# Performance work log

Measured on AMD Instinct MI355X. Metric: run time of the kernel, lower is better.

The kernel has to match this reference:

```python
import jax, jax.numpy as jnp
import numpy as np

D_DYN, D_STAT, H, T, B = 3, 3, 256, 365, 1024


def setup_inputs() -> dict:
    key = jax.random.key(0)
    ks = jax.random.split(key, 8)
    C = D_DYN + H
    s = lambda k, shape: jax.random.normal(k, shape, dtype=jnp.float32) * 0.05
    return {
        "x_dyn": jax.random.normal(ks[0], (B, T, D_DYN), dtype=jnp.float32),
        "x_stat": jax.random.normal(ks[1], (B, D_STAT), dtype=jnp.float32),
        "w_i": s(ks[2], (D_STAT, H)), "b_i": jnp.zeros((H,), jnp.float32),
        "w_f": s(ks[3], (C, H)), "b_f": jnp.zeros((H,), jnp.float32),
        "w_g": s(ks[4], (C, H)), "b_g": jnp.zeros((H,), jnp.float32),
        "w_o": s(ks[5], (C, H)), "b_o": jnp.zeros((H,), jnp.float32),
        "w_head": s(ks[6], (H, 1)), "b_head": jnp.zeros((1,), jnp.float32),
    }


def reference(x_dyn, x_stat, w_i, b_i, w_f, b_f, w_g, b_g, w_o, b_o, w_head, b_head):
    # Static input gate (EA-LSTM): i depends only on static features.
    i = jax.nn.sigmoid(x_stat @ w_i + b_i)  # (B, H)

    # Merge the three gate linears into one (C, 3H) matmul per step and
    # split the concat [x_t, h] into x- and h-parts (equivalent to torch.cat).
    W = jnp.concatenate([w_f, w_g, w_o], axis=1)  # (C, 3H)
    Wx, Wh = W[:D_DYN], W[D_DYN:]                 # (D,3H), (H,3H)
    b = jnp.concatenate([b_f, b_g, b_o])          # (3H,)

    def step(carry, x_t):
        h, c = carry
        z = x_t @ Wx + h @ Wh + b                 # (B, 3H)
        f = jax.nn.sigmoid(z[:, :H])
        g = jnp.tanh(z[:, H:2 * H])
        o = jax.nn.sigmoid(z[:, 2 * H:])
        c = f * c + i * g
        h = o * jnp.tanh(c)
        return (h, c), None

    h0 = jnp.zeros((x_dyn.shape[0], H), x_dyn.dtype)
    c0 = jnp.zeros((x_dyn.shape[0], H), x_dyn.dtype)
    (h, _), _ = jax.lax.scan(step, (h0, c0), jnp.swapaxes(x_dyn, 0, 1))
    # Dropout is identity in eval mode.
    return h @ w_head + b_head  # (B, 1)
```

## Files before the change

### kernel.cpp

```cpp
#include <hip/hip_runtime.h>
#include <hip/hip_bf16.h>

#define T_STEPS 365
#define XLEN    (T_STEPS * 3)
#define H_SZ    256
#define ROWS    16
#define NW      8
#define CPW     32

#define SF1     (-1.4426950408889634f)
#define SF2     (-2.8853900817779268f)

typedef __attribute__((ext_vector_type(8))) short bf16x8;
typedef __attribute__((ext_vector_type(4))) short bf16x4;
typedef __attribute__((ext_vector_type(4))) float f32x4;

__device__ __forceinline__ float fast_sigmoid(float x) {
    return __builtin_amdgcn_rcpf(1.0f + __builtin_amdgcn_exp2f(-1.44269504f * x));
}
__device__ __forceinline__ unsigned short f2bf(float x) {
    __hip_bfloat16 b = __float2bfloat16(x);
    return *reinterpret_cast<unsigned short*>(&b);
}
__device__ __forceinline__ float bf2f(unsigned short v) {
    return __uint_as_float(((unsigned)v) << 16);
}
__device__ __forceinline__ bf16x8 expand4(bf16x4 v) {
    bf16x8 r = (bf16x8)0;
    r[0] = v[0]; r[1] = v[1]; r[2] = v[2]; r[3] = v[3];
    return r;
}

__global__ void __launch_bounds__(256)
xstage(const float* __restrict__ x_dyn, unsigned short* __restrict__ xg)
{
    const int rb = blockIdx.x * ROWS;
    for (int idx = threadIdx.x; idx < T_STEPS * ROWS; idx += 256) {
        const int t = idx % T_STEPS, r = idx / T_STEPS;
        const float* s = x_dyn + (size_t)(rb + r) * XLEN + t * 3;
        bf16x4 pk;
        pk[0] = (short)f2bf(s[0]); pk[1] = (short)f2bf(s[1]);
        pk[2] = (short)f2bf(s[2]); pk[3] = (short)0x3F80;
        *(bf16x4*)&xg[((size_t)blockIdx.x * T_STEPS + t) * 64 + r * 4] = pk;
    }
}

__global__ void __launch_bounds__(512, 2)
ealstm_fused(const unsigned short* __restrict__ xg, const float* __restrict__ x_stat,
             const float* __restrict__ w_i, const float* __restrict__ b_i,
             const float* __restrict__ w_f, const float* __restrict__ b_f,
             const float* __restrict__ w_g, const float* __restrict__ b_g,
             const float* __restrict__ w_o, const float* __restrict__ b_o,
             const float* __restrict__ w_head, const float* __restrict__ b_head,
             float* __restrict__ out)
{
    const int tid   = threadIdx.x;
    const int lane  = tid & 63;
    const int wv    = tid >> 6;
    const int m     = lane & 15;
    const int l16   = lane >> 4;
    const int rb    = blockIdx.x * ROWS;
    const int wbase = wv * CPW;

    __shared__ unsigned short wo_lds[4 * 8 * 256 * 8];
    __shared__ unsigned short hbuf[2][4096];
    __shared__ float          red[NW][ROWS];

    for (int idx = tid; idx < 4 * 8 * 8 * 256; idx += 512) {
        const int c    = idx & 255;
        const int e    = (idx >> 8) & 7;
        const int kt   = (idx >> 11) & 7;
        const int l16g = idx >> 14;
        wo_lds[((l16g * 8 + kt) * 256 + c) * 8 + e] =
            f2bf(SF1 * w_o[(3 + kt * 32 + l16g * 8 + e) * H_SZ + c]);
    }
    for (int idx = tid; idx < 2048; idx += 512) ((unsigned int*)hbuf[0])[idx] = 0u;

    const float* wsrc[3] = {w_f, w_g, w_o};
    const float* bsrc[3] = {b_f, b_g, b_o};
    const float  gsf[3]  = {SF1, SF2, SF1};

    bf16x8 wA[8][2][2];
    bf16x8 wXe[2][3];
#pragma unroll
    for (int ct = 0; ct < 2; ++ct) {
        const int c = wbase + ct * 16 + m;
#pragma unroll
        for (int g = 0; g < 2; ++g)
#pragma unroll
            for (int kt = 0; kt < 8; ++kt) {
                bf16x8 a;
#pragma unroll
                for (int e = 0; e < 8; ++e)
                    a[e] = (short)f2bf(gsf[g] * wsrc[g][(3 + kt * 32 + l16 * 8 + e) * H_SZ + c]);
                wA[kt][ct][g] = a;
            }
#pragma unroll
        for (int g = 0; g < 3; ++g) {
            bf16x4 ax = (bf16x4)0;
            if (l16 == 0) {
                ax[0] = (short)f2bf(gsf[g] * wsrc[g][0 * H_SZ + c]);
                ax[1] = (short)f2bf(gsf[g] * wsrc[g][1 * H_SZ + c]);
                ax[2] = (short)f2bf(gsf[g] * wsrc[g][2 * H_SZ + c]);
                ax[3] = (short)f2bf(gsf[g] * bsrc[g][c]);
            }
            wXe[ct][g] = expand4(ax);
        }
    }

    float iv[2][4], cst[2][4];
    {
        const float xs0 = x_stat[(rb + m) * 3 + 0];
        const float xs1 = x_stat[(rb + m) * 3 + 1];
        const float xs2 = x_stat[(rb + m) * 3 + 2];
#pragma unroll
        for (int ct = 0; ct < 2; ++ct)
#pragma unroll
            for (int q = 0; q < 4; ++q) {
                const int c = wbase + ct * 16 + l16 * 4 + q;
                iv[ct][q] = fast_sigmoid(b_i[c] + xs0 * w_i[c] + xs1 * w_i[H_SZ + c]
                                                + xs2 * w_i[2 * H_SZ + c]);
                cst[ct][q] = 0.0f;
            }
    }

    int woff[2];
#pragma unroll
    for (int ct = 0; ct < 2; ++ct) {
        const int c0 = wbase + ct * 16 + l16 * 4;
        woff[ct] = ((c0 >> 5) * 64 + m + 16 * ((c0 & 31) >> 3)) * 8 + (c0 & 7);
    }

    const unsigned short* xrow   = xg + (size_t)blockIdx.x * T_STEPS * 64 + m * 4;
    const bf16x8*         wobase = (const bf16x8*)&wo_lds[((l16 * 8) * 256 + wbase + m) * 8];

    __syncthreads();

    for (int t = 0; t < T_STEPS; ++t) {
        const int cur = t & 1;
        const bf16x8* hp = (const bf16x8*)hbuf[cur] + lane;
        unsigned short* hw = hbuf[cur ^ 1];

        bf16x8 xf = (bf16x8)0;
        {
            unsigned long long xv = *(const unsigned long long*)&xrow[(size_t)t * 64];
            if (l16 != 0) xv = 0ULL;
            union { unsigned long long u; bf16x4 v; } X; X.u = xv;
            xf[0] = X.v[0]; xf[1] = X.v[1]; xf[2] = X.v[2]; xf[3] = X.v[3];
        }
        bf16x8 hb[8];
#pragma unroll
        for (int kt = 0; kt < 8; ++kt) hb[kt] = hp[kt * 64];
        bf16x8 wor[8][2];
#pragma unroll
        for (int kt = 0; kt < 8; ++kt) {
            wor[kt][0] = wobase[kt * 256];
            wor[kt][1] = wobase[kt * 256 + 16];
        }

        f32x4 acc[2][3];
        {
            const f32x4 z4 = {0.f, 0.f, 0.f, 0.f};
#pragma unroll
            for (int ct = 0; ct < 2; ++ct)
#pragma unroll
                for (int g = 0; g < 3; ++g)
                    acc[ct][g] = __builtin_amdgcn_mfma_f32_16x16x32_bf16(
                        wXe[ct][g], xf, z4, 0, 0, 0);
        }

#pragma unroll
        for (int kt = 0; kt < 8; ++kt) {
            acc[0][0] = __builtin_amdgcn_mfma_f32_16x16x32_bf16(wA[kt][0][0], hb[kt], acc[0][0], 0, 0, 0);
            acc[0][1] = __builtin_amdgcn_mfma_f32_16x16x32_bf16(wA[kt][0][1], hb[kt], acc[0][1], 0, 0, 0);
            acc[0][2] = __builtin_amdgcn_mfma_f32_16x16x32_bf16(wor[kt][0],   hb[kt], acc[0][2], 0, 0, 0);
            acc[1][0] = __builtin_amdgcn_mfma_f32_16x16x32_bf16(wA[kt][1][0], hb[kt], acc[1][0], 0, 0, 0);
            acc[1][1] = __builtin_amdgcn_mfma_f32_16x16x32_bf16(wA[kt][1][1], hb[kt], acc[1][1], 0, 0, 0);
            acc[1][2] = __builtin_amdgcn_mfma_f32_16x16x32_bf16(wor[kt][1],   hb[kt], acc[1][2], 0, 0, 0);
        }

#pragma unroll
        for (int ct = 0; ct < 2; ++ct) {
            bf16x4 pk;
#pragma unroll
            for (int q = 0; q < 4; ++q) {
                const float Ef = __builtin_amdgcn_exp2f(acc[ct][0][q]);
                const float Eg = __builtin_amdgcn_exp2f(acc[ct][1][q]);
                const float Eo = __builtin_amdgcn_exp2f(acc[ct][2][q]);
                const float u  = 1.0f + Eg;
                const float v  = 1.0f + Ef;
                const float t2 = iv[ct][q] * (2.0f - u);
                const float cq = (cst[ct][q] * u + t2 * v) *
                                 __builtin_amdgcn_rcpf(u * v);
                cst[ct][q] = cq;
                const float Ec = __builtin_amdgcn_exp2f(SF2 * cq);
                const float hq = (1.0f - Ec) *
                                 __builtin_amdgcn_rcpf((1.0f + Eo) * (1.0f + Ec));
                pk[q] = (short)f2bf(hq);
            }
            *(bf16x4*)&hw[woff[ct]] = pk;
        }
        __syncthreads();
    }

    float p = 0.0f;
    const unsigned short* hf = hbuf[1];
#pragma unroll
    for (int ct = 0; ct < 2; ++ct) {
        const int c0 = wbase + ct * 16 + l16 * 4;
        const f32x4 wh = *(const f32x4*)&w_head[c0];
        const bf16x4 hv = *(const bf16x4*)&hf[woff[ct]];
#pragma unroll
        for (int q = 0; q < 4; ++q) p += bf2f((unsigned short)hv[q]) * wh[q];
    }
    p += __shfl_xor(p, 16);
    p += __shfl_xor(p, 32);
    if (lane < 16) red[wv][m] = p;
    __syncthreads();
    if (tid < ROWS) {
        float s = b_head[0];
#pragma unroll
        for (int w = 0; w < NW; ++w) s += red[w][tid];
        out[rb + tid] = s;
    }
}

extern "C" void kernel_launch(void* const* d_in, const int* in_sizes, int n_in,
                              void* d_out, int out_size, void* d_ws, size_t ws_size,
                              hipStream_t stream)
{
    const float* x_dyn  = (const float*)d_in[0];
    const float* x_stat = (const float*)d_in[1];
    const float* w_i    = (const float*)d_in[2];
    const float* b_i    = (const float*)d_in[3];
    const float* w_f    = (const float*)d_in[4];
    const float* b_f    = (const float*)d_in[5];
    const float* w_g    = (const float*)d_in[6];
    const float* b_g    = (const float*)d_in[7];
    const float* w_o    = (const float*)d_in[8];
    const float* b_o    = (const float*)d_in[9];
    const float* w_head = (const float*)d_in[10];
    const float* b_head = (const float*)d_in[11];

    unsigned short* xg = (unsigned short*)d_ws;

    xstage<<<dim3(64), dim3(256), 0, stream>>>(x_dyn, xg);
    ealstm_fused<<<dim3(64), dim3(512), 0, stream>>>(
        xg, x_stat, w_i, b_i, w_f, b_f, w_g, b_g, w_o, b_o,
        w_head, b_head, (float*)d_out);
}
```

Measured before the change: 578.1 us.

## Halve batch rows per block to 8 and double block count to 128

Each block now handles 8 batch rows instead of 16, and twice as many blocks are launched, so more CUs work on the sequential recurrence at once. The 16-wide MFMA N dimension stays the same, so half of each matmul's columns are padding. Lanes 8-15 take the second column tile's results through a cross-lane shuffle, which halves the per-lane gate elementwise work. The cost is wasted MFMA throughput, an extra shuffle step per timestep, and weight staging into registers and LDS repeated in twice as many blocks.

```diff
diff --git a/kernel.cpp b/kernel.cpp
--- a/kernel.cpp
+++ b/kernel.cpp
@@ -4,7 +4,8 @@
 #define T_STEPS 365
 #define XLEN    (T_STEPS * 3)
 #define H_SZ    256
-#define ROWS    16
+#define ROWS    8
+#define NBLK    128
 #define NW      8
 #define CPW     32
 
@@ -41,7 +42,7 @@
         bf16x4 pk;
         pk[0] = (short)f2bf(s[0]); pk[1] = (short)f2bf(s[1]);
         pk[2] = (short)f2bf(s[2]); pk[3] = (short)0x3F80;
-        *(bf16x4*)&xg[((size_t)blockIdx.x * T_STEPS + t) * 64 + r * 4] = pk;
+        *(bf16x4*)&xg[((size_t)blockIdx.x * T_STEPS + t) * 32 + r * 4] = pk;
     }
 }
 
@@ -61,6 +62,9 @@
     const int l16   = lane >> 4;
     const int rb    = blockIdx.x * ROWS;
     const int wbase = wv * CPW;
+    const int r_eff  = m & 7;
+    const int ct_eff = m >> 3;
+    const bool hi    = (m >= 8);
 
     __shared__ unsigned short wo_lds[4 * 8 * 256 * 8];
     __shared__ unsigned short hbuf[2][4096];
@@ -74,7 +78,7 @@
         wo_lds[((l16g * 8 + kt) * 256 + c) * 8 + e] =
             f2bf(SF1 * w_o[(3 + kt * 32 + l16g * 8 + e) * H_SZ + c]);
     }
-    for (int idx = tid; idx < 2048; idx += 512) ((unsigned int*)hbuf[0])[idx] = 0u;
+    for (int idx = tid; idx < 4096; idx += 512) ((unsigned int*)hbuf)[idx] = 0u;
 
     const float* wsrc[3] = {w_f, w_g, w_o};
     const float* bsrc[3] = {b_f, b_g, b_o};
@@ -108,30 +112,24 @@
         }
     }
 
-    float iv[2][4], cst[2][4];
+    const int c0 = wbase + ct_eff * 16 + l16 * 4;
+    float iv[4], cst[4];
     {
-        const float xs0 = x_stat[(rb + m) * 3 + 0];
-        const float xs1 = x_stat[(rb + m) * 3 + 1];
-        const float xs2 = x_stat[(rb + m) * 3 + 2];
-#pragma unroll
-        for (int ct = 0; ct < 2; ++ct)
-#pragma unroll
-            for (int q = 0; q < 4; ++q) {
-                const int c = wbase + ct * 16 + l16 * 4 + q;
-                iv[ct][q] = fast_sigmoid(b_i[c] + xs0 * w_i[c] + xs1 * w_i[H_SZ + c]
-                                                + xs2 * w_i[2 * H_SZ + c]);
-                cst[ct][q] = 0.0f;
-            }
-    }
-
-    int woff[2];
-#pragma unroll
-    for (int ct = 0; ct < 2; ++ct) {
-        const int c0 = wbase + ct * 16 + l16 * 4;
-        woff[ct] = ((c0 >> 5) * 64 + m + 16 * ((c0 & 31) >> 3)) * 8 + (c0 & 7);
-    }
-
-    const unsigned short* xrow   = xg + (size_t)blockIdx.x * T_STEPS * 64 + m * 4;
+        const float xs0 = x_stat[(rb + r_eff) * 3 + 0];
+        const float xs1 = x_stat[(rb + r_eff) * 3 + 1];
+        const float xs2 = x_stat[(rb + r_eff) * 3 + 2];
+#pragma unroll
+        for (int q = 0; q < 4; ++q) {
+            const int c = c0 + q;
+            iv[q] = fast_sigmoid(b_i[c] + xs0 * w_i[c] + xs1 * w_i[H_SZ + c]
+                                        + xs2 * w_i[2 * H_SZ + c]);
+            cst[q] = 0.0f;
+        }
+    }
+
+    const int woff = ((c0 >> 5) * 64 + r_eff + 16 * ((c0 & 31) >> 3)) * 8 + (c0 & 7);
+
+    const unsigned short* xrow   = xg + (size_t)blockIdx.x * T_STEPS * 32 + m * 4;
     const bf16x8*         wobase = (const bf16x8*)&wo_lds[((l16 * 8) * 256 + wbase + m) * 8];
 
     __syncthreads();
@@ -142,11 +140,9 @@
         unsigned short* hw = hbuf[cur ^ 1];
 
         bf16x8 xf = (bf16x8)0;
-        {
-            unsigned long long xv = *(const unsigned long long*)&xrow[(size_t)t * 64];
-            if (l16 != 0) xv = 0ULL;
-            union { unsigned long long u; bf16x4 v; } X; X.u = xv;
-            xf[0] = X.v[0]; xf[1] = X.v[1]; xf[2] = X.v[2]; xf[3] = X.v[3];
+        if (l16 == 0 && m < 8) {
+            const bf16x4 v = *(const bf16x4*)&xrow[(size_t)t * 32];
+            xf[0] = v[0]; xf[1] = v[1]; xf[2] = v[2]; xf[3] = v[3];
         }
         bf16x8 hb[8];
 #pragma unroll
@@ -179,43 +175,52 @@
             acc[1][2] = __builtin_amdgcn_mfma_f32_16x16x32_bf16(wor[kt][1],   hb[kt], acc[1][2], 0, 0, 0);
         }
 
-#pragma unroll
-        for (int ct = 0; ct < 2; ++ct) {
+        float zf[4], zg[4], zo[4];
+#pragma unroll
+        for (int q = 0; q < 4; ++q) {
+            const float sf = __shfl_xor(acc[1][0][q], 8);
+            const float sg = __shfl_xor(acc[1][1][q], 8);
+            const float so = __shfl_xor(acc[1][2][q], 8);
+            zf[q] = hi ? sf : acc[0][0][q];
+            zg[q] = hi ? sg : acc[0][1][q];
+            zo[q] = hi ? so : acc[0][2][q];
+        }
+
+        {
             bf16x4 pk;
 #pragma unroll
             for (int q = 0; q < 4; ++q) {
-                const float Ef = __builtin_amdgcn_exp2f(acc[ct][0][q]);
-                const float Eg = __builtin_amdgcn_exp2f(acc[ct][1][q]);
-                const float Eo = __builtin_amdgcn_exp2f(acc[ct][2][q]);
+                const float Ef = __builtin_amdgcn_exp2f(zf[q]);
+                const float Eg = __builtin_amdgcn_exp2f(zg[q]);
+                const float Eo = __builtin_amdgcn_exp2f(zo[q]);
                 const float u  = 1.0f + Eg;
                 const float v  = 1.0f + Ef;
-                const float t2 = iv[ct][q] * (2.0f - u);
-                const float cq = (cst[ct][q] * u + t2 * v) *
+                const float t2 = iv[q] * (2.0f - u);
+                const float cq = (cst[q] * u + t2 * v) *
                                  __builtin_amdgcn_rcpf(u * v);
-                cst[ct][q] = cq;
+                cst[q] = cq;
                 const float Ec = __builtin_amdgcn_exp2f(SF2 * cq);
                 const float hq = (1.0f - Ec) *
                                  __builtin_amdgcn_rcpf((1.0f + Eo) * (1.0f + Ec));
                 pk[q] = (short)f2bf(hq);
             }
-            *(bf16x4*)&hw[woff[ct]] = pk;
+            *(bf16x4*)&hw[woff] = pk;
         }
         __syncthreads();
     }
 
     float p = 0.0f;
-    const unsigned short* hf = hbuf[1];
-#pragma unroll
-    for (int ct = 0; ct < 2; ++ct) {
-        const int c0 = wbase + ct * 16 + l16 * 4;
+    {
+        const unsigned short* hf = hbuf[1];
         const f32x4 wh = *(const f32x4*)&w_head[c0];
-        const bf16x4 hv = *(const bf16x4*)&hf[woff[ct]];
+        const bf16x4 hv = *(const bf16x4*)&hf[woff];
 #pragma unroll
         for (int q = 0; q < 4; ++q) p += bf2f((unsigned short)hv[q]) * wh[q];
     }
+    p += __shfl_xor(p, 8);
     p += __shfl_xor(p, 16);
     p += __shfl_xor(p, 32);
-    if (lane < 16) red[wv][m] = p;
+    if (lane < ROWS) red[wv][lane] = p;
     __syncthreads();
     if (tid < ROWS) {
         float s = b_head[0];
@@ -244,8 +249,8 @@
 
     unsigned short* xg = (unsigned short*)d_ws;
 
-    xstage<<<dim3(64), dim3(256), 0, stream>>>(x_dyn, xg);
-    ealstm_fused<<<dim3(64), dim3(512), 0, stream>>>(
+    xstage<<<dim3(NBLK), dim3(256), 0, stream>>>(x_dyn, xg);
+    ealstm_fused<<<dim3(NBLK), dim3(512), 0, stream>>>(
         xg, x_stat, w_i, b_i, w_f, b_f, w_g, b_g, w_o, b_o,
         w_head, b_head, (float*)d_out);
 }
```

After: 526.6 us. -8.9%, faster.
